# Kernel optimization log

Measured on AMD Instinct MI355X. Metric: run time of the kernel, lower is better.

The kernel has to match this reference:

```python
import jax, jax.numpy as jnp
import numpy as np

WS = 7        # window_size
NH = 12       # num_heads
HD = 32       # head_dim
SCALE = HD ** -0.5


def _rel_pos_index(ws: int) -> np.ndarray:
    # Static [N, N] index into the (2ws-1)^2 relative position bias table.
    coords = np.stack(np.meshgrid(np.arange(ws), np.arange(ws), indexing='ij'))
    coords = coords.reshape(2, -1)                       # [2, N]
    rel = coords[:, :, None] - coords[:, None, :]        # [2, N, N]
    rel = rel.transpose(1, 2, 0).copy()                  # [N, N, 2]
    rel[:, :, 0] += ws - 1
    rel[:, :, 1] += ws - 1
    rel[:, :, 0] *= 2 * ws - 1
    return rel.sum(-1)                                   # [N, N]

_REL_IDX = jnp.asarray(_rel_pos_index(WS))


def setup_inputs() -> dict:
    key = jax.random.key(0)
    ks = jax.random.split(key, 7)
    BW, N, C = 2048, WS * WS, 384
    nW = 64
    return {
        'x': jax.random.normal(ks[0], (BW, N, C), jnp.float32),
        'mask': jax.random.normal(ks[1], (nW, N, N), jnp.float32),
        'qkv_w': jax.random.normal(ks[2], (3 * C, C), jnp.float32) * 0.02,
        'qkv_b': jax.random.normal(ks[3], (3 * C,), jnp.float32) * 0.02,
        'proj_w': jax.random.normal(ks[4], (C, C), jnp.float32) * 0.02,
        'proj_b': jax.random.normal(ks[5], (C,), jnp.float32) * 0.02,
        'bias_table': jax.random.normal(ks[6], ((2 * WS - 1) ** 2, NH), jnp.float32) * 0.02,
    }


def reference(x, mask, qkv_w, qkv_b, proj_w, proj_b, bias_table):
    BW, N, C = x.shape
    # qkv projection: [BW, N, 3, H, hd]
    qkv = (x @ qkv_w.T + qkv_b).reshape(BW, N, 3, NH, HD)
    qkv = jnp.transpose(qkv, (2, 0, 3, 1, 4))            # [3, BW, H, N, hd]
    q, k, v = qkv[0], qkv[1], qkv[2]
    attn = jnp.einsum('bhnd,bhmd->bhnm', q, k) * SCALE   # [BW, H, N, N]
    # gathered relative position bias: [N, N, H] -> [H, N, N]
    bias = bias_table[_REL_IDX]                          # [N, N, H]
    attn = attn + jnp.transpose(bias, (2, 0, 1))[None]
    # shifted-window mask add: [nW, N, N] broadcast over batch and heads
    nW = mask.shape[0]
    attn = attn.reshape(BW // nW, nW, NH, N, N) + mask[None, :, None]
    attn = attn.reshape(BW, NH, N, N)
    attn = jax.nn.softmax(attn, axis=-1)
    out = jnp.einsum('bhnm,bhmd->bhnd', attn, v)         # [BW, H, N, hd]
    out = jnp.transpose(out, (0, 2, 1, 3)).reshape(BW, N, C)
    return out @ proj_w.T + proj_b
```

## Files before the change

kernel.cpp:

```cpp
#include <hip/hip_runtime.h>

typedef __attribute__((ext_vector_type(4))) float f32x4;
typedef __attribute__((ext_vector_type(8))) short s16x8;

#define MFMA16(a, b, c) __builtin_amdgcn_mfma_f32_16x16x32_bf16(a, b, c, 0, 0, 0)

static __device__ __forceinline__ unsigned short f2b(float f) {
  unsigned int u = __float_as_uint(f);
  u += 0x7fff + ((u >> 16) & 1);
  return (unsigned short)(u >> 16);
}

static __device__ __forceinline__ void gload_lds16(const unsigned short* g, unsigned short* l) {
  __builtin_amdgcn_global_load_lds(
      (const __attribute__((address_space(1))) unsigned int*)g,
      (__attribute__((address_space(3))) unsigned int*)l, 16, 0, 0);
}

#define BW    2048
#define NTOK  49
#define CDIM  384
#define NHEAD 12
#define HDIM  32
#define NWIN  64
#define MROWS (BW * NTOK)
#define SCALE 0.17677669529663687f

#define OFF_X    ((size_t)0)
#define OFF_QKV  ((size_t)77070336)
#define OFF_QW   ((size_t)308281344)
#define OFF_PW   ((size_t)309166080)
#define OFF_COMB ((size_t)309460992)

__global__ __launch_bounds__(256) void cast_kernel(const float* __restrict__ src,
                                                   unsigned short* __restrict__ dst, int n4) {
  int i = blockIdx.x * 256 + threadIdx.x;
  if (i >= n4) return;
  float4 f = ((const float4*)src)[i];
  ushort4 o;
  o.x = f2b(f.x); o.y = f2b(f.y); o.z = f2b(f.z); o.w = f2b(f.w);
  ((ushort4*)dst)[i] = o;
}

__global__ __launch_bounds__(256) void build_comb(const float* __restrict__ mask,
                                                  const float* __restrict__ bias_table,
                                                  float* __restrict__ comb) {
  int idx = blockIdx.x * 256 + threadIdx.x;
  if (idx >= NWIN * NHEAD * NTOK * NTOK) return;
  int ij = idx % (NTOK * NTOK);
  int wh = idx / (NTOK * NTOK);
  int h = wh % NHEAD;
  int w = wh / NHEAD;
  int i = ij / NTOK, j = ij % NTOK;
  int yi = i / 7, xi = i % 7, yj = j / 7, xj = j % 7;
  int rel = (yi - yj + 6) * 13 + (xi - xj + 6);
  comb[idx] = mask[w * (NTOK * NTOK) + ij] + bias_table[rel * NHEAD + h];
}

template <bool OUT_BF16>
__global__ __launch_bounds__(256) void gemm_bt(const unsigned short* __restrict__ A,
                                               const unsigned short* __restrict__ Bt,
                                               const float* __restrict__ bias,
                                               void* __restrict__ Cv,
                                               int M, int N, int K) {
  __shared__ __align__(16) unsigned short As[128 * 32];
  __shared__ __align__(16) unsigned short Bs[128 * 32];
  const int tid = threadIdx.x;
  const int lane = tid & 63;
  const int wave = tid >> 6;
  const int lr = lane & 15, lg = lane >> 4;
  const int wm = (wave >> 1) * 64, wn = (wave & 1) * 64;
  const size_t tileM = (size_t)blockIdx.y * 128;
  const size_t tileN = (size_t)blockIdx.x * 128;

  const unsigned short* Ab = A + tileM * K;
  const unsigned short* Bb = Bt + tileN * K;

  const int c0 = tid, c1 = tid + 256;
  const size_t a0 = (size_t)(c0 >> 2) * K + (c0 & 3) * 8;
  const size_t a1 = (size_t)(c1 >> 2) * K + (c1 & 3) * 8;

  f32x4 acc[4][4] = {};

  for (int k0 = 0; k0 < K; k0 += 32) {
    gload_lds16(Ab + a0 + k0, As + c0 * 8);
    gload_lds16(Ab + a1 + k0, As + c1 * 8);
    gload_lds16(Bb + a0 + k0, Bs + c0 * 8);
    gload_lds16(Bb + a1 + k0, Bs + c1 * 8);
    __syncthreads();
    s16x8 af[4], bf[4];
#pragma unroll
    for (int mt = 0; mt < 4; ++mt)
      af[mt] = *(const s16x8*)&As[(wm + mt * 16 + lr) * 32 + lg * 8];
#pragma unroll
    for (int nt = 0; nt < 4; ++nt)
      bf[nt] = *(const s16x8*)&Bs[(wn + nt * 16 + lr) * 32 + lg * 8];
#pragma unroll
    for (int mt = 0; mt < 4; ++mt)
#pragma unroll
      for (int nt = 0; nt < 4; ++nt)
        acc[mt][nt] = MFMA16(af[mt], bf[nt], acc[mt][nt]);
    __syncthreads();
  }

  unsigned short* Cb = (unsigned short*)Cv;
  float* Cf = (float*)Cv;
#pragma unroll
  for (int nt = 0; nt < 4; ++nt) {
    const size_t gcol = tileN + wn + nt * 16 + lr;
    const float bv = bias[gcol];
#pragma unroll
    for (int mt = 0; mt < 4; ++mt)
#pragma unroll
      for (int r = 0; r < 4; ++r) {
        const size_t grow = tileM + wm + mt * 16 + lg * 4 + r;
        const float v = acc[mt][nt][r] + bv;
        if (OUT_BF16) Cb[grow * (size_t)N + gcol] = f2b(v);
        else          Cf[grow * (size_t)N + gcol] = v;
      }
  }
}

#define PSTR 72
__global__ __launch_bounds__(64) void attn_kernel(const unsigned short* __restrict__ qkv,
                                                  const float* __restrict__ comb,
                                                  unsigned short* __restrict__ out) {
  __shared__ __align__(16) unsigned short Pt[64 * PSTR];
  __shared__ __align__(16) unsigned short VT[32 * PSTR];
  const int b = blockIdx.x;
  const int h = blockIdx.y;
  const int lane = threadIdx.x;
  const int lr = lane & 15, lg = lane >> 4;
  const unsigned short* base = qkv + (size_t)b * NTOK * (3 * CDIM) + h * HDIM;

  for (int i = lane; i < (32 * PSTR) / 8; i += 64) {
    s16x8 z;
#pragma unroll
    for (int j = 0; j < 8; ++j) z[j] = 0;
    *(s16x8*)&VT[i * 8] = z;
  }
  __syncthreads();

  for (int c = lane; c < NTOK * 4; c += 64) {
    int k = c % NTOK;
    int dg = c / NTOK;
    s16x8 v = *(const s16x8*)(base + 2 * CDIM + (size_t)k * (3 * CDIM) + dg * 8);
#pragma unroll
    for (int j = 0; j < 8; ++j) VT[(dg * 8 + j) * PSTR + k] = v[j];
  }

  s16x8 qf[4], kf[4];
#pragma unroll
  for (int mt = 0; mt < 4; ++mt) {
    int t = mt * 16 + lr;
    if (t < NTOK) {
      qf[mt] = *(const s16x8*)(base + (size_t)t * (3 * CDIM) + lg * 8);
      kf[mt] = *(const s16x8*)(base + CDIM + (size_t)t * (3 * CDIM) + lg * 8);
    } else {
#pragma unroll
      for (int j = 0; j < 8; ++j) { qf[mt][j] = 0; kf[mt][j] = 0; }
    }
  }

  f32x4 S[4][4] = {};
#pragma unroll
  for (int mt = 0; mt < 4; ++mt)
#pragma unroll
    for (int nt = 0; nt < 4; ++nt)
      S[mt][nt] = MFMA16(qf[mt], kf[nt], S[mt][nt]);

  const float* cb = comb + ((size_t)(b & 63) * NHEAD + h) * (NTOK * NTOK);

#pragma unroll
  for (int mt = 0; mt < 4; ++mt) {
#pragma unroll
    for (int r = 0; r < 4; ++r) {
      const int row = mt * 16 + lg * 4 + r;
      const bool rowok = row < NTOK;
      float sv[4];
      float mx = -1e30f;
#pragma unroll
      for (int nt = 0; nt < 4; ++nt) {
        const int col = nt * 16 + lr;
        float s;
        if (col < NTOK)
          s = rowok ? S[mt][nt][r] * SCALE + cb[row * NTOK + col] : 0.0f;
        else
          s = -1e30f;
        sv[nt] = s;
        mx = fmaxf(mx, s);
      }
#pragma unroll
      for (int off = 8; off; off >>= 1) mx = fmaxf(mx, __shfl_xor(mx, off, 16));
      float sum = 0.f;
#pragma unroll
      for (int nt = 0; nt < 4; ++nt) {
        float e = exp2f((sv[nt] - mx) * 1.4426950408889634f);
        sv[nt] = e;
        sum += e;
      }
#pragma unroll
      for (int off = 8; off; off >>= 1) sum += __shfl_xor(sum, off, 16);
      const float inv = 1.0f / sum;
#pragma unroll
      for (int nt = 0; nt < 4; ++nt)
        Pt[row * PSTR + nt * 16 + lr] = f2b(sv[nt] * inv);
    }
  }
  __syncthreads();

  f32x4 O[4][2] = {};
#pragma unroll
  for (int ks = 0; ks < 2; ++ks) {
    s16x8 pf[4], vf[2];
#pragma unroll
    for (int mt = 0; mt < 4; ++mt)
      pf[mt] = *(const s16x8*)&Pt[(mt * 16 + lr) * PSTR + ks * 32 + lg * 8];
#pragma unroll
    for (int n2 = 0; n2 < 2; ++n2)
      vf[n2] = *(const s16x8*)&VT[(n2 * 16 + lr) * PSTR + ks * 32 + lg * 8];
#pragma unroll
    for (int mt = 0; mt < 4; ++mt)
#pragma unroll
      for (int n2 = 0; n2 < 2; ++n2)
        O[mt][n2] = MFMA16(pf[mt], vf[n2], O[mt][n2]);
  }

  unsigned short* ob = out + (size_t)b * NTOK * CDIM + h * HDIM;
#pragma unroll
  for (int mt = 0; mt < 4; ++mt)
#pragma unroll
    for (int r = 0; r < 4; ++r) {
      const int row = mt * 16 + lg * 4 + r;
      if (row < NTOK) {
#pragma unroll
        for (int n2 = 0; n2 < 2; ++n2)
          ob[(size_t)row * CDIM + n2 * 16 + lr] = f2b(O[mt][n2][r]);
      }
    }
}

extern "C" void kernel_launch(void* const* d_in, const int* in_sizes, int n_in,
                              void* d_out, int out_size, void* d_ws, size_t ws_size,
                              hipStream_t stream) {
  const float* x          = (const float*)d_in[0];
  const float* mask       = (const float*)d_in[1];
  const float* qkv_w      = (const float*)d_in[2];
  const float* qkv_b      = (const float*)d_in[3];
  const float* proj_w     = (const float*)d_in[4];
  const float* proj_b     = (const float*)d_in[5];
  const float* bias_table = (const float*)d_in[6];
  float* out = (float*)d_out;
  char* ws = (char*)d_ws;

  unsigned short* xb   = (unsigned short*)(ws + OFF_X);
  unsigned short* qkvb = (unsigned short*)(ws + OFF_QKV);
  unsigned short* qw   = (unsigned short*)(ws + OFF_QW);
  unsigned short* pw   = (unsigned short*)(ws + OFF_PW);
  float* comb          = (float*)(ws + OFF_COMB);

  cast_kernel<<<(MROWS * CDIM / 4 + 255) / 256, 256, 0, stream>>>(x, xb, MROWS * CDIM / 4);
  cast_kernel<<<(3 * CDIM * CDIM / 4 + 255) / 256, 256, 0, stream>>>(qkv_w, qw, 3 * CDIM * CDIM / 4);
  cast_kernel<<<(CDIM * CDIM / 4 + 255) / 256, 256, 0, stream>>>(proj_w, pw, CDIM * CDIM / 4);

  {
    int n = NWIN * NHEAD * NTOK * NTOK;
    build_comb<<<(n + 255) / 256, 256, 0, stream>>>(mask, bias_table, comb);
  }

  gemm_bt<true><<<dim3((3 * CDIM) / 128, MROWS / 128), 256, 0, stream>>>(
      xb, qw, qkv_b, qkvb, MROWS, 3 * CDIM, CDIM);

  attn_kernel<<<dim3(BW, NHEAD), 64, 0, stream>>>(qkvb, comb, xb);

  gemm_bt<false><<<dim3(CDIM / 128, MROWS / 128), 256, 0, stream>>>(
      xb, pw, proj_b, out, MROWS, CDIM, CDIM);
}
```

Measured before the change: 755.7 us.

## Emit head-major Q/K and pre-transposed V from QKV GEMM epilogue

```diff
diff --git a/kernel.cpp b/kernel.cpp
--- a/kernel.cpp
+++ b/kernel.cpp
@@ -25,12 +25,14 @@
 #define NWIN  64
 #define MROWS (BW * NTOK)
 #define SCALE 0.17677669529663687f
+#define QK_ELEMS ((size_t)BW * NHEAD * NTOK * HDIM)
 
 #define OFF_X    ((size_t)0)
-#define OFF_QKV  ((size_t)77070336)
-#define OFF_QW   ((size_t)308281344)
-#define OFF_PW   ((size_t)309166080)
-#define OFF_COMB ((size_t)309460992)
+#define OFF_Q    ((size_t)77070336)
+#define OFF_K    ((size_t)154140672)
+#define OFF_QW   ((size_t)231211008)
+#define OFF_PW   ((size_t)232095744)
+#define OFF_COMB ((size_t)232390656)
 
 __global__ __launch_bounds__(256) void cast_kernel(const float* __restrict__ src,
                                                    unsigned short* __restrict__ dst, int n4) {
@@ -57,11 +59,12 @@
   comb[idx] = mask[w * (NTOK * NTOK) + ij] + bias_table[rel * NHEAD + h];
 }
 
-template <bool OUT_BF16>
+template <int MODE>
 __global__ __launch_bounds__(256) void gemm_bt(const unsigned short* __restrict__ A,
                                                const unsigned short* __restrict__ Bt,
                                                const float* __restrict__ bias,
                                                void* __restrict__ Cv,
+                                               unsigned short* __restrict__ vtb,
                                                int M, int N, int K) {
   __shared__ __align__(16) unsigned short As[128 * 32];
   __shared__ __align__(16) unsigned short Bs[128 * 32];
@@ -103,63 +106,66 @@
     __syncthreads();
   }
 
-  unsigned short* Cb = (unsigned short*)Cv;
-  float* Cf = (float*)Cv;
-#pragma unroll
-  for (int nt = 0; nt < 4; ++nt) {
-    const size_t gcol = tileN + wn + nt * 16 + lr;
-    const float bv = bias[gcol];
+  if (MODE == 0) {
+    float* Cf = (float*)Cv;
+#pragma unroll
+    for (int nt = 0; nt < 4; ++nt) {
+      const size_t gcol = tileN + wn + nt * 16 + lr;
+      const float bv = bias[gcol];
+#pragma unroll
+      for (int mt = 0; mt < 4; ++mt)
+#pragma unroll
+        for (int r = 0; r < 4; ++r) {
+          const size_t grow = tileM + wm + mt * 16 + lg * 4 + r;
+          Cf[grow * (size_t)N + gcol] = acc[mt][nt][r] + bv;
+        }
+    }
+  } else {
+    unsigned short* qko = (unsigned short*)Cv;
+    const int which = blockIdx.x / 3;
 #pragma unroll
     for (int mt = 0; mt < 4; ++mt)
 #pragma unroll
       for (int r = 0; r < 4; ++r) {
-        const size_t grow = tileM + wm + mt * 16 + lg * 4 + r;
-        const float v = acc[mt][nt][r] + bv;
-        if (OUT_BF16) Cb[grow * (size_t)N + gcol] = f2b(v);
-        else          Cf[grow * (size_t)N + gcol] = v;
+        const int grow = (int)tileM + wm + mt * 16 + lg * 4 + r;
+        const int b = grow / 49;
+        const int t = grow - b * 49;
+#pragma unroll
+        for (int nt = 0; nt < 4; ++nt) {
+          const int gcol = (int)tileN + wn + nt * 16 + lr;
+          const int cc = gcol - which * 384;
+          const int hh = cc >> 5, d = cc & 31;
+          const float v = acc[mt][nt][r] + bias[gcol];
+          const size_t bh = (size_t)b * NHEAD + hh;
+          if (which == 2) vtb[(bh * HDIM + d) * 64 + t] = f2b(v);
+          else            qko[(size_t)which * QK_ELEMS + (bh * NTOK + t) * HDIM + d] = f2b(v);
+        }
       }
   }
 }
 
 #define PSTR 72
-__global__ __launch_bounds__(64) void attn_kernel(const unsigned short* __restrict__ qkv,
+__global__ __launch_bounds__(64) void attn_kernel(const unsigned short* __restrict__ q,
+                                                  const unsigned short* __restrict__ k,
+                                                  const unsigned short* __restrict__ vt,
                                                   const float* __restrict__ comb,
                                                   unsigned short* __restrict__ out) {
   __shared__ __align__(16) unsigned short Pt[64 * PSTR];
-  __shared__ __align__(16) unsigned short VT[32 * PSTR];
   const int b = blockIdx.x;
   const int h = blockIdx.y;
   const int lane = threadIdx.x;
   const int lr = lane & 15, lg = lane >> 4;
-  const unsigned short* base = qkv + (size_t)b * NTOK * (3 * CDIM) + h * HDIM;
-
-  for (int i = lane; i < (32 * PSTR) / 8; i += 64) {
-    s16x8 z;
-#pragma unroll
-    for (int j = 0; j < 8; ++j) z[j] = 0;
-    *(s16x8*)&VT[i * 8] = z;
-  }
-  __syncthreads();
-
-  for (int c = lane; c < NTOK * 4; c += 64) {
-    int k = c % NTOK;
-    int dg = c / NTOK;
-    s16x8 v = *(const s16x8*)(base + 2 * CDIM + (size_t)k * (3 * CDIM) + dg * 8);
-#pragma unroll
-    for (int j = 0; j < 8; ++j) VT[(dg * 8 + j) * PSTR + k] = v[j];
-  }
+  const size_t bh = (size_t)b * NHEAD + h;
+  const unsigned short* qb = q + bh * (NTOK * HDIM);
+  const unsigned short* kb = k + bh * (NTOK * HDIM);
+  const unsigned short* vb = vt + bh * (HDIM * 64);
 
   s16x8 qf[4], kf[4];
 #pragma unroll
   for (int mt = 0; mt < 4; ++mt) {
-    int t = mt * 16 + lr;
-    if (t < NTOK) {
-      qf[mt] = *(const s16x8*)(base + (size_t)t * (3 * CDIM) + lg * 8);
-      kf[mt] = *(const s16x8*)(base + CDIM + (size_t)t * (3 * CDIM) + lg * 8);
-    } else {
-#pragma unroll
-      for (int j = 0; j < 8; ++j) { qf[mt][j] = 0; kf[mt][j] = 0; }
-    }
+    const int off = (mt * 16 + lr) * HDIM + lg * 8;
+    qf[mt] = *(const s16x8*)(qb + off);
+    kf[mt] = *(const s16x8*)(kb + off);
   }
 
   f32x4 S[4][4] = {};
@@ -218,7 +224,7 @@
       pf[mt] = *(const s16x8*)&Pt[(mt * 16 + lr) * PSTR + ks * 32 + lg * 8];
 #pragma unroll
     for (int n2 = 0; n2 < 2; ++n2)
-      vf[n2] = *(const s16x8*)&VT[(n2 * 16 + lr) * PSTR + ks * 32 + lg * 8];
+      vf[n2] = *(const s16x8*)(vb + (n2 * 16 + lr) * 64 + ks * 32 + lg * 8);
 #pragma unroll
     for (int mt = 0; mt < 4; ++mt)
 #pragma unroll
@@ -254,10 +260,12 @@
   char* ws = (char*)d_ws;
 
   unsigned short* xb   = (unsigned short*)(ws + OFF_X);
-  unsigned short* qkvb = (unsigned short*)(ws + OFF_QKV);
+  unsigned short* qb   = (unsigned short*)(ws + OFF_Q);
+  unsigned short* kb   = (unsigned short*)(ws + OFF_K);
   unsigned short* qw   = (unsigned short*)(ws + OFF_QW);
   unsigned short* pw   = (unsigned short*)(ws + OFF_PW);
   float* comb          = (float*)(ws + OFF_COMB);
+  unsigned short* vtb  = (unsigned short*)d_out;
 
   cast_kernel<<<(MROWS * CDIM / 4 + 255) / 256, 256, 0, stream>>>(x, xb, MROWS * CDIM / 4);
   cast_kernel<<<(3 * CDIM * CDIM / 4 + 255) / 256, 256, 0, stream>>>(qkv_w, qw, 3 * CDIM * CDIM / 4);
@@ -268,11 +276,11 @@
     build_comb<<<(n + 255) / 256, 256, 0, stream>>>(mask, bias_table, comb);
   }
 
-  gemm_bt<true><<<dim3((3 * CDIM) / 128, MROWS / 128), 256, 0, stream>>>(
-      xb, qw, qkv_b, qkvb, MROWS, 3 * CDIM, CDIM);
-
-  attn_kernel<<<dim3(BW, NHEAD), 64, 0, stream>>>(qkvb, comb, xb);
-
-  gemm_bt<false><<<dim3(CDIM / 128, MROWS / 128), 256, 0, stream>>>(
-      xb, pw, proj_b, out, MROWS, CDIM, CDIM);
-}
+  gemm_bt<2><<<dim3((3 * CDIM) / 128, MROWS / 128), 256, 0, stream>>>(
+      xb, qw, qkv_b, qb, vtb, MROWS, 3 * CDIM, CDIM);
+
+  attn_kernel<<<dim3(BW, NHEAD), 64, 0, stream>>>(qb, kb, vtb, comb, xb);
+
+  gemm_bt<0><<<dim3(CDIM / 128, MROWS / 128), 256, 0, stream>>>(
+      xb, pw, proj_b, out, nullptr, MROWS, CDIM, CDIM);
+}
```

New measurement: 764.5 us. No clear change (+1.2%).
